# Kernel tuning notes

Measured on AMD Instinct MI355X. Metric: run time of the kernel, lower is better.

## Reference

```python
import jax, jax.numpy as jnp
import numpy as np

B, I, H, O = 4096, 1024, 2048, 512  # batch, input_size, experts_out(hidden), experts_hidden(output)
E_SPEC, E_SH = 4, 4


def _experts(x, W1, b1, W2, b2):
    # x:[B,I], W1:[E,I,H], b1:[E,H], W2:[E,H,O], b2:[E,O] -> [E,B,O]
    # Expert: fc2(dropout(relu(fc1(x)))); dropout is identity in eval mode.
    h = jax.nn.relu(jnp.einsum('bi,eih->ebh', x, W1) + b1[:, None, :])
    return jnp.einsum('ebh,eho->ebo', h, W2) + b2[:, None, :]


def setup_inputs() -> dict:
    key = jax.random.key(0)
    ks = jax.random.split(key, 32)
    s = 0.02
    d = {}
    d['x_shared'] = jax.random.normal(ks[0], (B, I), jnp.float32)
    d['x_task1'] = jax.random.normal(ks[1], (B, I), jnp.float32)
    d['x_task2'] = jax.random.normal(ks[2], (B, I), jnp.float32)
    # expert params for shared / task1 / task2 groups
    for n, (grp, kbase) in enumerate([('sh', 3), ('t1', 8), ('t2', 13)]):
        E = E_SH if grp == 'sh' else E_SPEC
        d[f'w1_{grp}'] = jax.random.normal(ks[kbase], (E, I, H), jnp.float32) * s
        d[f'b1_{grp}'] = jnp.zeros((E, H), jnp.float32)
        d[f'w2_{grp}'] = jax.random.normal(ks[kbase + 1], (E, H, O), jnp.float32) * s
        d[f'b2_{grp}'] = jnp.zeros((E, O), jnp.float32)
    # gate params
    d['wg_sh'] = jax.random.normal(ks[20], (I, 2 * E_SPEC + E_SH), jnp.float32) * s
    d['bg_sh'] = jnp.zeros((2 * E_SPEC + E_SH,), jnp.float32)
    d['wg_t1'] = jax.random.normal(ks[21], (I, E_SPEC + E_SH), jnp.float32) * s
    d['bg_t1'] = jnp.zeros((E_SPEC + E_SH,), jnp.float32)
    d['wg_t2'] = jax.random.normal(ks[22], (I, E_SPEC + E_SH), jnp.float32) * s
    d['bg_t2'] = jnp.zeros((E_SPEC + E_SH,), jnp.float32)
    return d


def reference(x_shared, x_task1, x_task2,
              w1_sh, b1_sh, w2_sh, b2_sh,
              w1_t1, b1_t1, w2_t1, b2_t1,
              w1_t2, b1_t2, w2_t2, b2_t2,
              wg_sh, bg_sh, wg_t1, bg_t1, wg_t2, bg_t2):
    sh_o = _experts(x_shared, w1_sh, b1_sh, w2_sh, b2_sh)  # [Esh,B,O]
    t1_o = _experts(x_task1, w1_t1, b1_t1, w2_t1, b2_t1)   # [Esp,B,O]
    t2_o = _experts(x_task2, w1_t2, b1_t2, w2_t2, b2_t2)   # [Esp,B,O]

    g1 = jax.nn.softmax(x_task1 @ wg_t1 + bg_t1, axis=1)    # [B,Esp+Esh]
    g2 = jax.nn.softmax(x_task2 @ wg_t2 + bg_t2, axis=1)
    gs = jax.nn.softmax(x_shared @ wg_sh + bg_sh, axis=1)   # [B,2Esp+Esh]

    out1 = jnp.einsum('ebc,be->bc', jnp.concatenate([t1_o, sh_o], 0), g1)
    out2 = jnp.einsum('ebc,be->bc', jnp.concatenate([t2_o, sh_o], 0), g2)
    out_sh = jnp.einsum('ebc,be->bc', jnp.concatenate([t1_o, t2_o, sh_o], 0), gs)
    # if_last=False -> return [shared, task1, task2]
    return (out_sh, out1, out2)
```

## Files before the change

### kernel.cpp

```cpp
#include <hip/hip_runtime.h>

#define B_DIM 4096
#define I_DIM 1024
#define H_DIM 2048
#define O_DIM 512

typedef unsigned short ushort_t;
typedef unsigned long long ull_t;
typedef __attribute__((ext_vector_type(4))) float f32x4;
typedef __attribute__((ext_vector_type(8))) short bf16x8;
typedef __attribute__((ext_vector_type(8))) unsigned short u16x8;
typedef __attribute__((ext_vector_type(4))) unsigned short u16x4;

__device__ __forceinline__ unsigned short f2bf(float f) {
  union { float f; unsigned int u; } v; v.f = f;
  unsigned int u = v.u;
  u += 0x7fffu + ((u >> 16) & 1u);
  return (unsigned short)(u >> 16);
}
__device__ __forceinline__ float bf2f(unsigned short h) {
  union { unsigned int u; float f; } v; v.u = ((unsigned int)h) << 16;
  return v.f;
}

__device__ __forceinline__ void gld16(const void* g, void* l) {
  __builtin_amdgcn_global_load_lds(
      (const __attribute__((address_space(1))) unsigned int*)((ull_t)g),
      (__attribute__((address_space(3))) unsigned int*)((unsigned int)(ull_t)l),
      16, 0, 0);
}

__device__ __forceinline__ int swz_off(int row, int col) {
  int off = ((((row >> 4) << 1) + (col >> 5)) << 10) + ((row & 15) << 6) + ((col & 31) << 1);
  off ^= ((row >> 3) & 1) << 5;
  return off;
}

template <bool RELU, int WM, int WN, int MR, int NR>
__device__ __forceinline__ void gemm_core(
    const ushort_t* __restrict__ A,
    const ushort_t* __restrict__ Bt,
    const float*    __restrict__ bias,
    ushort_t*       __restrict__ C,
    int N, int K, int bm0, int bn0)
{
  constexpr int BM = WM * MR * 16;
  constexpr int BN = WN * NR * 16;
  constexpr int CA = BM / 64;
  constexpr int CB = BN / 64;
  constexpr int NTH = WM * WN * 64;
  constexpr int MH = MR / 2, NH = NR / 2;
  constexpr int ABYTES = BM * 128;
  constexpr int BBYTES = BN * 128;
  constexpr int VM = CA + CB;

  __shared__ __align__(16) char lds[2 * (ABYTES + BBYTES)];

  const int tid  = threadIdx.x;
  const int lane = tid & 63;
  const int wave = tid >> 6;
  const int wm = wave / WN, wn = wave % WN;
  const int r16 = lane & 15, kq = lane >> 4;

  int loffA[CA]; ull_t goffA[CA];
  int loffB[CB]; ull_t goffB[CB];
#pragma unroll
  for (int r = 0; r < CA; ++r) {
    const int L = (r * NTH + tid) * 16;
    const int P = L ^ (((L >> 9) & 1) << 5);
    const int s = P >> 10;
    const int row = ((s >> 1) << 4) | ((P >> 6) & 15);
    const int col = ((s & 1) << 5) | (((P >> 4) & 3) << 3);
    loffA[r] = L;
    goffA[r] = (ull_t)(bm0 + row) * K + col;
  }
#pragma unroll
  for (int r = 0; r < CB; ++r) {
    const int L = (r * NTH + tid) * 16;
    const int P = L ^ (((L >> 9) & 1) << 5);
    const int s = P >> 10;
    const int row = ((s >> 1) << 4) | ((P >> 6) & 15);
    const int col = ((s & 1) << 5) | (((P >> 4) & 3) << 3);
    loffB[r] = L;
    goffB[r] = (ull_t)(bn0 + row) * K + col;
  }
  const int NT = K >> 6;

  int offA[MR][2], offB[NR][2];
#pragma unroll
  for (int m = 0; m < MR; ++m)
#pragma unroll
    for (int ks = 0; ks < 2; ++ks)
      offA[m][ks] = swz_off(wm * MR * 16 + m * 16 + r16, ks * 32 + kq * 8);
#pragma unroll
  for (int n = 0; n < NR; ++n)
#pragma unroll
    for (int ks = 0; ks < 2; ++ks)
      offB[n][ks] = swz_off(wn * NR * 16 + n * 16 + r16, ks * 32 + kq * 8);

  f32x4 acc[MR][NR] = {};

  auto stageA = [&](int b, int kt) {
    char* base = lds + b * (ABYTES + BBYTES);
    const int k0 = kt << 6;
#pragma unroll
    for (int r = 0; r < CA; ++r) gld16(A + goffA[r] + k0, base + loffA[r]);
  };
  auto stageB = [&](int b, int kt) {
    char* base = lds + b * (ABYTES + BBYTES) + ABYTES;
    const int k0 = kt << 6;
#pragma unroll
    for (int r = 0; r < CB; ++r) gld16(Bt + goffB[r] + k0, base + loffB[r]);
  };

  stageA(0, 0); stageB(0, 0);
  stageA(1, 1); stageB(1, 1);

  for (int kt = 0; kt < NT; ++kt) {
    const int b = kt & 1;
    const bool pre = (kt + 2 < NT);
    if (kt < NT - 1) {
      if constexpr (VM == 8)      asm volatile("s_waitcnt vmcnt(8)" ::: "memory");
      else if constexpr (VM == 6) asm volatile("s_waitcnt vmcnt(6)" ::: "memory");
      else                        asm volatile("s_waitcnt vmcnt(0)" ::: "memory");
    } else                        asm volatile("s_waitcnt vmcnt(0)" ::: "memory");
    __builtin_amdgcn_s_barrier();

    const char* tA = lds + b * (ABYTES + BBYTES);
    const char* tB = tA + ABYTES;

    bf16x8 a_lo[MH][2], a_hi[MH][2], b_lo[NH][2], b_hi[NH][2];

#pragma unroll
    for (int m = 0; m < MH; ++m) {
      a_lo[m][0] = *(const bf16x8*)(tA + offA[m][0]);
      a_lo[m][1] = *(const bf16x8*)(tA + offA[m][1]);
    }
#pragma unroll
    for (int n = 0; n < NH; ++n) {
      b_lo[n][0] = *(const bf16x8*)(tB + offB[n][0]);
      b_lo[n][1] = *(const bf16x8*)(tB + offB[n][1]);
    }
    asm volatile("s_waitcnt lgkmcnt(0)" ::: "memory");
    __builtin_amdgcn_sched_barrier(0);
    __builtin_amdgcn_s_setprio(1);
#pragma unroll
    for (int m = 0; m < MH; ++m)
#pragma unroll
      for (int n = 0; n < NH; ++n)
#pragma unroll
        for (int ks = 0; ks < 2; ++ks)
          acc[m][n] = __builtin_amdgcn_mfma_f32_16x16x32_bf16(a_lo[m][ks], b_lo[n][ks], acc[m][n], 0, 0, 0);
    __builtin_amdgcn_s_setprio(0);

#pragma unroll
    for (int n = 0; n < NH; ++n) {
      b_hi[n][0] = *(const bf16x8*)(tB + offB[n + NH][0]);
      b_hi[n][1] = *(const bf16x8*)(tB + offB[n + NH][1]);
    }
    asm volatile("s_waitcnt lgkmcnt(0)" ::: "memory");
    __builtin_amdgcn_sched_barrier(0);
    __builtin_amdgcn_s_setprio(1);
#pragma unroll
    for (int m = 0; m < MH; ++m)
#pragma unroll
      for (int n = 0; n < NH; ++n)
#pragma unroll
        for (int ks = 0; ks < 2; ++ks)
          acc[m][n + NH] = __builtin_amdgcn_mfma_f32_16x16x32_bf16(a_lo[m][ks], b_hi[n][ks], acc[m][n + NH], 0, 0, 0);
    __builtin_amdgcn_s_setprio(0);
    asm volatile("" ::: "memory");
    __builtin_amdgcn_s_barrier();

#pragma unroll
    for (int m = 0; m < MH; ++m) {
      a_hi[m][0] = *(const bf16x8*)(tA + offA[m + MH][0]);
      a_hi[m][1] = *(const bf16x8*)(tA + offA[m + MH][1]);
    }
    if (pre) stageB(b, kt + 2);
    asm volatile("s_waitcnt lgkmcnt(0)" ::: "memory");
    __builtin_amdgcn_sched_barrier(0);
    __builtin_amdgcn_s_setprio(1);
#pragma unroll
    for (int m = 0; m < MH; ++m)
#pragma unroll
      for (int n = 0; n < NH; ++n)
#pragma unroll
        for (int ks = 0; ks < 2; ++ks)
          acc[m + MH][n + NH] = __builtin_amdgcn_mfma_f32_16x16x32_bf16(a_hi[m][ks], b_hi[n][ks], acc[m + MH][n + NH], 0, 0, 0);
    __builtin_amdgcn_s_setprio(0);
    asm volatile("" ::: "memory");
    __builtin_amdgcn_s_barrier();

    if (pre) stageA(b, kt + 2);
    __builtin_amdgcn_sched_barrier(0);
    __builtin_amdgcn_s_setprio(1);
#pragma unroll
    for (int m = 0; m < MH; ++m)
#pragma unroll
      for (int n = 0; n < NH; ++n)
#pragma unroll
        for (int ks = 0; ks < 2; ++ks)
          acc[m + MH][n] = __builtin_amdgcn_mfma_f32_16x16x32_bf16(a_hi[m][ks], b_lo[n][ks], acc[m + MH][n], 0, 0, 0);
    __builtin_amdgcn_s_setprio(0);
  }

  float bv[NR];
#pragma unroll
  for (int n = 0; n < NR; ++n) bv[n] = bias[bn0 + wn * NR * 16 + n * 16 + r16];
#pragma unroll
  for (int m = 0; m < MR; ++m) {
    const int row = bm0 + wm * MR * 16 + m * 16 + kq * 4;
#pragma unroll
    for (int n = 0; n < NR; ++n) {
      const int col = bn0 + wn * NR * 16 + n * 16 + r16;
#pragma unroll
      for (int j = 0; j < 4; ++j) {
        float v = acc[m][n][j] + bv[n];
        if (RELU) v = fmaxf(v, 0.f);
        C[(ull_t)(row + j) * N + col] = f2bf(v);
      }
    }
  }
}

__device__ __forceinline__ void xcd_swz(int& bx, int& by, int& bz) {
  const int gx = gridDim.x, gy = gridDim.y;
  const int total = gx * gy * gridDim.z;
  const int flat = blockIdx.x + gx * (blockIdx.y + gy * blockIdx.z);
  const int q = total >> 3;
  const int s = (flat & 7) * q + (flat >> 3);
  bx = s % gx;
  const int rest = s / gx;
  by = rest % gy;
  bz = rest / gy;
}

__global__ __launch_bounds__(512, 2) void gemm1_256_kernel(
    const ushort_t* __restrict__ xb,
    const ushort_t* __restrict__ w1t,
    const float* __restrict__ b1_t1, const float* __restrict__ b1_t2, const float* __restrict__ b1_sh,
    ushort_t* __restrict__ hbuf,
    int ebase)
{
  int bx, by, bz; xcd_swz(bx, by, bz);
  const int eg = ebase + bz;
  const ushort_t* A  = xb + (ull_t)(eg >> 2) * B_DIM * I_DIM;
  const ushort_t* Bt = w1t + (ull_t)bz * H_DIM * I_DIM;
  const float* bias = (eg < 4 ? b1_t1 : eg < 8 ? b1_t2 : b1_sh) + (ull_t)(eg & 3) * H_DIM;
  ushort_t* C = hbuf + (ull_t)bz * B_DIM * H_DIM;
  gemm_core<true, 2, 4, 8, 4>(A, Bt, bias, C, H_DIM, I_DIM, by * 256, bx * 256);
}

__global__ __launch_bounds__(512, 2) void gemm2_256_kernel(
    const ushort_t* __restrict__ hbuf,
    const ushort_t* __restrict__ w2t,
    const float* __restrict__ b2_t1, const float* __restrict__ b2_t2, const float* __restrict__ b2_sh,
    ushort_t* __restrict__ eout,
    int ebase)
{
  int bx, by, bz; xcd_swz(bx, by, bz);
  const int eg = ebase + bz;
  const ushort_t* A  = hbuf + (ull_t)bz * B_DIM * H_DIM;
  const ushort_t* Bt = w2t + (ull_t)bz * O_DIM * H_DIM;
  const float* bias = (eg < 4 ? b2_t1 : eg < 8 ? b2_t2 : b2_sh) + (ull_t)(eg & 3) * O_DIM;
  ushort_t* C = eout + (ull_t)eg * B_DIM * O_DIM;
  gemm_core<false, 4, 2, 4, 4>(A, Bt, bias, C, O_DIM, H_DIM, by * 256, bx * 128);
}

__global__ void tcast64_kernel(const float* __restrict__ s_t1, const float* __restrict__ s_t2,
                               const float* __restrict__ s_sh, ushort_t* __restrict__ dst,
                               int R, int C, int ebase)
{
  __shared__ float tile[64][33];
  const int eg = ebase + blockIdx.z;
  const float* src = (eg < 4 ? s_t1 : eg < 8 ? s_t2 : s_sh) + (ull_t)(eg & 3) * R * C;
  ushort_t* d = dst + (ull_t)blockIdx.z * R * C;
  const int tx = threadIdx.x, ty = threadIdx.y;
  const int r0 = blockIdx.y * 64, c0 = blockIdx.x * 32;
#pragma unroll
  for (int i = 0; i < 64; i += 8)
    tile[i + ty][tx] = src[(ull_t)(r0 + i + ty) * C + c0 + tx];
  __syncthreads();
  const int tid = ty * 32 + tx;
  const int c = tid >> 3, q = tid & 7;
  u16x8 rv;
#pragma unroll
  for (int k = 0; k < 8; ++k) rv[k] = f2bf(tile[q * 8 + k][c]);
  *(u16x8*)(d + (ull_t)(c0 + c) * R + r0 + q * 8) = rv;
}

__global__ void cast_x_kernel(const float* __restrict__ xt1, const float* __restrict__ xt2,
                              const float* __restrict__ xsh, ushort_t* __restrict__ dst)
{
  const int slot = blockIdx.y;
  const float* src = slot == 0 ? xt1 : slot == 1 ? xt2 : xsh;
  const ull_t base = ((ull_t)blockIdx.x * 256 + threadIdx.x) * 8;
  const f32x4* s4 = (const f32x4*)(src + base);
  f32x4 a = s4[0], b = s4[1];
  u16x8 r;
  r[0] = f2bf(a[0]); r[1] = f2bf(a[1]); r[2] = f2bf(a[2]); r[3] = f2bf(a[3]);
  r[4] = f2bf(b[0]); r[5] = f2bf(b[1]); r[6] = f2bf(b[2]); r[7] = f2bf(b[3]);
  *(u16x8*)(dst + (ull_t)slot * B_DIM * I_DIM + base) = r;
}

__global__ void prep_gates_w_kernel(const float* __restrict__ wg_sh, const float* __restrict__ wg_t1,
                                    const float* __restrict__ wg_t2, ushort_t* __restrict__ wgtb)
{
  const int t = blockIdx.x;
  const float* src = t == 0 ? wg_sh : t == 1 ? wg_t1 : wg_t2;
  const int n = t == 0 ? 12 : 8;
  ushort_t* dst = wgtb + (ull_t)t * 16 * I_DIM;
  for (int i = threadIdx.x; i < 16 * (I_DIM / 8); i += blockDim.x) {
    const int c = i >> 7, j0 = (i & 127) * 8;
    u16x8 r;
#pragma unroll
    for (int k = 0; k < 8; ++k)
      r[k] = (c < n) ? f2bf(src[(ull_t)(j0 + k) * n + c]) : (ushort_t)0;
    *(u16x8*)(dst + (ull_t)c * I_DIM + j0) = r;
  }
}

__global__ __launch_bounds__(256, 2) void gates_mfma_kernel(
    const ushort_t* __restrict__ xb, const ushort_t* __restrict__ wgtb,
    const float* __restrict__ bg_sh, const float* __restrict__ bg_t1, const float* __restrict__ bg_t2,
    float* __restrict__ gates)
{
  __shared__ __align__(16) ushort_t As[128 * 32];
  const int task = blockIdx.y;
  const int slot = task == 0 ? 2 : task - 1;
  const int n = task == 0 ? 12 : 8;
  const float* bg = task == 0 ? bg_sh : task == 1 ? bg_t1 : bg_t2;
  float* out = task == 0 ? gates
             : task == 1 ? gates + (ull_t)B_DIM * 12
                         : gates + (ull_t)B_DIM * 20;
  const ushort_t* A  = xb + (ull_t)slot * B_DIM * I_DIM;
  const ushort_t* Bt = wgtb + (ull_t)task * 16 * I_DIM;

  const int tid = threadIdx.x, lane = tid & 63, wave = tid >> 6;
  const int brow = blockIdx.x * 128;
  const int r16 = lane & 15, kq = lane >> 4;

  f32x4 acc[2] = {};
  const int c0 = tid, c1 = tid + 256;
  const ull_t a_off0 = (ull_t)(brow + (c0 >> 2)) * I_DIM + (c0 & 3) * 8;
  const ull_t a_off1 = (ull_t)(brow + (c1 >> 2)) * I_DIM + (c1 & 3) * 8;

  for (int k0 = 0; k0 < I_DIM; k0 += 32) {
    gld16(A + a_off0 + k0, As + c0 * 8);
    gld16(A + a_off1 + k0, As + c1 * 8);
    __syncthreads();
    const bf16x8 bfr = *(const bf16x8*)(Bt + (ull_t)r16 * I_DIM + k0 + kq * 8);
    const bf16x8 af0 = *(const bf16x8*)(As + (wave * 32 + r16) * 32 + kq * 8);
    const bf16x8 af1 = *(const bf16x8*)(As + (wave * 32 + 16 + r16) * 32 + kq * 8);
    acc[0] = __builtin_amdgcn_mfma_f32_16x16x32_bf16(af0, bfr, acc[0], 0, 0, 0);
    acc[1] = __builtin_amdgcn_mfma_f32_16x16x32_bf16(af1, bfr, acc[1], 0, 0, 0);
    __syncthreads();
  }

  const float bv = (r16 < n) ? bg[r16] : 0.f;
#pragma unroll
  for (int m = 0; m < 2; ++m) {
#pragma unroll
    for (int j = 0; j < 4; ++j) {
      float v = (r16 < n) ? (acc[m][j] + bv) : -1e30f;
      float mx = v;
#pragma unroll
      for (int d = 1; d < 16; d <<= 1) mx = fmaxf(mx, __shfl_xor(mx, d));
      const float e = __expf(v - mx);
      float s = e;
#pragma unroll
      for (int d = 1; d < 16; d <<= 1) s += __shfl_xor(s, d);
      const int row = brow + wave * 32 + m * 16 + kq * 4 + j;
      if (r16 < n) out[(ull_t)row * n + r16] = e / s;
    }
  }
}

__global__ __launch_bounds__(256) void combine_kernel(
    const ushort_t* __restrict__ eout, const float* __restrict__ gates, float* __restrict__ out)
{
  const ull_t idx4 = (ull_t)blockIdx.x * 256 + threadIdx.x;
  const int b  = (int)(idx4 >> 7);
  const int o4 = ((int)idx4 & 127) * 4;
  const float* gs = gates + (ull_t)b * 12;
  const float* g1 = gates + (ull_t)B_DIM * 12 + (ull_t)b * 8;
  const float* g2 = gates + (ull_t)B_DIM * 20 + (ull_t)b * 8;
  float osh[4] = {0, 0, 0, 0}, o1[4] = {0, 0, 0, 0}, o2[4] = {0, 0, 0, 0};
#pragma unroll
  for (int j = 0; j < 12; ++j) {
    const u16x4 ev = *(const u16x4*)(eout + ((ull_t)j * B_DIM + b) * O_DIM + o4);
    const float wsh = gs[j];
    const float w1 = (j < 4) ? g1[j] : (j >= 8 ? g1[j - 4] : 0.f);
    const float w2 = (j < 4) ? 0.f : g2[j - 4];
#pragma unroll
    for (int t = 0; t < 4; ++t) {
      const float e = bf2f(ev[t]);
      osh[t] += wsh * e; o1[t] += w1 * e; o2[t] += w2 * e;
    }
  }
  const ull_t nBO = (ull_t)B_DIM * O_DIM;
  const ull_t obase = (ull_t)b * O_DIM + o4;
  f32x4 v0 = {osh[0], osh[1], osh[2], osh[3]};
  f32x4 v1 = {o1[0], o1[1], o1[2], o1[3]};
  f32x4 v2 = {o2[0], o2[1], o2[2], o2[3]};
  *(f32x4*)(out + obase) = v0;
  *(f32x4*)(out + nBO + obase) = v1;
  *(f32x4*)(out + 2 * nBO + obase) = v2;
}

extern "C" void kernel_launch(void* const* d_in, const int* in_sizes, int n_in,
                              void* d_out, int out_size, void* d_ws, size_t ws_size,
                              hipStream_t stream)
{
  const float* x_sh  = (const float*)d_in[0];
  const float* x_t1  = (const float*)d_in[1];
  const float* x_t2  = (const float*)d_in[2];
  const float* w1_sh = (const float*)d_in[3];
  const float* b1_sh = (const float*)d_in[4];
  const float* w2_sh = (const float*)d_in[5];
  const float* b2_sh = (const float*)d_in[6];
  const float* w1_t1 = (const float*)d_in[7];
  const float* b1_t1 = (const float*)d_in[8];
  const float* w2_t1 = (const float*)d_in[9];
  const float* b2_t1 = (const float*)d_in[10];
  const float* w1_t2 = (const float*)d_in[11];
  const float* b1_t2 = (const float*)d_in[12];
  const float* w2_t2 = (const float*)d_in[13];
  const float* b2_t2 = (const float*)d_in[14];
  const float* wg_sh = (const float*)d_in[15];
  const float* bg_sh = (const float*)d_in[16];
  const float* wg_t1 = (const float*)d_in[17];
  const float* bg_t1 = (const float*)d_in[18];
  const float* wg_t2 = (const float*)d_in[19];
  const float* bg_t2 = (const float*)d_in[20];

  char* p = (char*)d_ws;
  auto alloc = [&](size_t bytes) { char* r = p; p += (bytes + 255) & ~(size_t)255; return r; };

  ushort_t* xb    = (ushort_t*)alloc(3ull * B_DIM * I_DIM * 2);
  ushort_t* eout  = (ushort_t*)alloc(12ull * B_DIM * O_DIM * 2);
  float*    gates = (float*)alloc(28ull * B_DIM * 4);
  ushort_t* wgtb  = (ushort_t*)alloc(3ull * 16 * I_DIM * 2);

  const size_t used_fixed = (size_t)(p - (char*)d_ws);
  const size_t per_e = ((size_t)H_DIM * I_DIM + (size_t)O_DIM * H_DIM + (size_t)B_DIM * H_DIM) * 2 + 3 * 256;
  int eb = 1;
  if (ws_size > used_fixed + per_e) eb = (int)((ws_size - used_fixed) / per_e);
  if (eb > 12) eb = 12;
  if (eb < 1)  eb = 1;

  ushort_t* w1t  = (ushort_t*)alloc((size_t)eb * H_DIM * I_DIM * 2);
  ushort_t* w2t  = (ushort_t*)alloc((size_t)eb * O_DIM * H_DIM * 2);
  ushort_t* hbuf = (ushort_t*)alloc((size_t)eb * B_DIM * H_DIM * 2);

  cast_x_kernel<<<dim3(2048, 3), 256, 0, stream>>>(x_t1, x_t2, x_sh, xb);
  prep_gates_w_kernel<<<3, 256, 0, stream>>>(wg_sh, wg_t1, wg_t2, wgtb);
  gates_mfma_kernel<<<dim3(B_DIM / 128, 3), 256, 0, stream>>>(xb, wgtb, bg_sh, bg_t1, bg_t2, gates);
  for (int ebase = 0; ebase < 12; ebase += eb) {
    const int cnt = (12 - ebase < eb) ? (12 - ebase) : eb;
    tcast64_kernel<<<dim3(H_DIM / 32, I_DIM / 64, cnt), dim3(32, 8), 0, stream>>>(
        w1_t1, w1_t2, w1_sh, w1t, I_DIM, H_DIM, ebase);
    tcast64_kernel<<<dim3(O_DIM / 32, H_DIM / 64, cnt), dim3(32, 8), 0, stream>>>(
        w2_t1, w2_t2, w2_sh, w2t, H_DIM, O_DIM, ebase);
    gemm1_256_kernel<<<dim3(H_DIM / 256, B_DIM / 256, cnt), 512, 0, stream>>>(
        xb, w1t, b1_t1, b1_t2, b1_sh, hbuf, ebase);
    gemm2_256_kernel<<<dim3(O_DIM / 128, B_DIM / 256, cnt), 512, 0, stream>>>(
        hbuf, w2t, b2_t1, b2_t2, b2_sh, eout, ebase);
  }
  combine_kernel<<<dim3((B_DIM * O_DIM / 4) / 256), 256, 0, stream>>>(eout, gates, (float*)d_out);
}
```

Before: 416.1 us.

## Retile gemm2 to 128x128, merge prefetch stages, simplify gates and widen combine

Changes several unrelated things at once. gemm2 moves to 128x128 tiles with 256-thread blocks, giving more blocks for the small-N second GEMM, and the per-thread load counts are now derived from tile bytes. In the shared GEMM core, one mid-iteration barrier is removed and both the A and B prefetches are issued together after the final barrier. The gates kernel drops its LDS staging and loads MFMA operands straight from global memory with two accumulators, and the combine kernel processes 8 elements per thread. The trade-off is less compute/load overlap inside each K-tile, in return for fewer barriers and better occupancy of the second GEMM.

Measured after the change: 414.5 us. No clear change (-0.4%).

```diff
diff --git a/kernel.cpp b/kernel.cpp
--- a/kernel.cpp
+++ b/kernel.cpp
@@ -46,12 +46,12 @@
 {
   constexpr int BM = WM * MR * 16;
   constexpr int BN = WN * NR * 16;
-  constexpr int CA = BM / 64;
-  constexpr int CB = BN / 64;
   constexpr int NTH = WM * WN * 64;
   constexpr int MH = MR / 2, NH = NR / 2;
   constexpr int ABYTES = BM * 128;
   constexpr int BBYTES = BN * 128;
+  constexpr int CA = ABYTES / (NTH * 16);
+  constexpr int CB = BBYTES / (NTH * 16);
   constexpr int VM = CA + CB;
 
   __shared__ __align__(16) char lds[2 * (ABYTES + BBYTES)];
@@ -120,10 +120,11 @@
     const int b = kt & 1;
     const bool pre = (kt + 2 < NT);
     if (kt < NT - 1) {
-      if constexpr (VM == 8)      asm volatile("s_waitcnt vmcnt(8)" ::: "memory");
-      else if constexpr (VM == 6) asm volatile("s_waitcnt vmcnt(6)" ::: "memory");
-      else                        asm volatile("s_waitcnt vmcnt(0)" ::: "memory");
-    } else                        asm volatile("s_waitcnt vmcnt(0)" ::: "memory");
+      static_assert(VM == 8, "vmcnt literal assumes 8 loads/K-tile/thread");
+      asm volatile("s_waitcnt vmcnt(8)" ::: "memory");
+    } else {
+      asm volatile("s_waitcnt vmcnt(0)" ::: "memory");
+    }
     __builtin_amdgcn_s_barrier();
 
     const char* tA = lds + b * (ABYTES + BBYTES);
@@ -169,15 +170,12 @@
         for (int ks = 0; ks < 2; ++ks)
           acc[m][n + NH] = __builtin_amdgcn_mfma_f32_16x16x32_bf16(a_lo[m][ks], b_hi[n][ks], acc[m][n + NH], 0, 0, 0);
     __builtin_amdgcn_s_setprio(0);
-    asm volatile("" ::: "memory");
-    __builtin_amdgcn_s_barrier();
 
 #pragma unroll
     for (int m = 0; m < MH; ++m) {
       a_hi[m][0] = *(const bf16x8*)(tA + offA[m + MH][0]);
       a_hi[m][1] = *(const bf16x8*)(tA + offA[m + MH][1]);
     }
-    if (pre) stageB(b, kt + 2);
     asm volatile("s_waitcnt lgkmcnt(0)" ::: "memory");
     __builtin_amdgcn_sched_barrier(0);
     __builtin_amdgcn_s_setprio(1);
@@ -192,7 +190,7 @@
     asm volatile("" ::: "memory");
     __builtin_amdgcn_s_barrier();
 
-    if (pre) stageA(b, kt + 2);
+    if (pre) { stageB(b, kt + 2); stageA(b, kt + 2); }
     __builtin_amdgcn_sched_barrier(0);
     __builtin_amdgcn_s_setprio(1);
 #pragma unroll
@@ -252,7 +250,7 @@
   gemm_core<true, 2, 4, 8, 4>(A, Bt, bias, C, H_DIM, I_DIM, by * 256, bx * 256);
 }
 
-__global__ __launch_bounds__(512, 2) void gemm2_256_kernel(
+__global__ __launch_bounds__(256, 2) void gemm2_128_kernel(
     const ushort_t* __restrict__ hbuf,
     const ushort_t* __restrict__ w2t,
     const float* __restrict__ b2_t1, const float* __restrict__ b2_t2, const float* __restrict__ b2_sh,
@@ -265,7 +263,7 @@
   const ushort_t* Bt = w2t + (ull_t)bz * O_DIM * H_DIM;
   const float* bias = (eg < 4 ? b2_t1 : eg < 8 ? b2_t2 : b2_sh) + (ull_t)(eg & 3) * O_DIM;
   ushort_t* C = eout + (ull_t)eg * B_DIM * O_DIM;
-  gemm_core<false, 4, 2, 4, 4>(A, Bt, bias, C, O_DIM, H_DIM, by * 256, bx * 128);
+  gemm_core<false, 2, 2, 4, 4>(A, Bt, bias, C, O_DIM, H_DIM, by * 128, bx * 128);
 }
 
 __global__ void tcast64_kernel(const float* __restrict__ s_t1, const float* __restrict__ s_t2,
@@ -321,12 +319,11 @@
   }
 }
 
-__global__ __launch_bounds__(256, 2) void gates_mfma_kernel(
+__global__ __launch_bounds__(256) void gates_direct_kernel(
     const ushort_t* __restrict__ xb, const ushort_t* __restrict__ wgtb,
     const float* __restrict__ bg_sh, const float* __restrict__ bg_t1, const float* __restrict__ bg_t2,
     float* __restrict__ gates)
 {
-  __shared__ __align__(16) ushort_t As[128 * 32];
   const int task = blockIdx.y;
   const int slot = task == 0 ? 2 : task - 1;
   const int n = task == 0 ? 12 : 8;
@@ -334,79 +331,74 @@
   float* out = task == 0 ? gates
              : task == 1 ? gates + (ull_t)B_DIM * 12
                          : gates + (ull_t)B_DIM * 20;
-  const ushort_t* A  = xb + (ull_t)slot * B_DIM * I_DIM;
-  const ushort_t* Bt = wgtb + (ull_t)task * 16 * I_DIM;
-
-  const int tid = threadIdx.x, lane = tid & 63, wave = tid >> 6;
-  const int brow = blockIdx.x * 128;
+
+  const int lane = threadIdx.x & 63, wave = threadIdx.x >> 6;
   const int r16 = lane & 15, kq = lane >> 4;
-
-  f32x4 acc[2] = {};
-  const int c0 = tid, c1 = tid + 256;
-  const ull_t a_off0 = (ull_t)(brow + (c0 >> 2)) * I_DIM + (c0 & 3) * 8;
-  const ull_t a_off1 = (ull_t)(brow + (c1 >> 2)) * I_DIM + (c1 & 3) * 8;
-
-  for (int k0 = 0; k0 < I_DIM; k0 += 32) {
-    gld16(A + a_off0 + k0, As + c0 * 8);
-    gld16(A + a_off1 + k0, As + c1 * 8);
-    __syncthreads();
-    const bf16x8 bfr = *(const bf16x8*)(Bt + (ull_t)r16 * I_DIM + k0 + kq * 8);
-    const bf16x8 af0 = *(const bf16x8*)(As + (wave * 32 + r16) * 32 + kq * 8);
-    const bf16x8 af1 = *(const bf16x8*)(As + (wave * 32 + 16 + r16) * 32 + kq * 8);
-    acc[0] = __builtin_amdgcn_mfma_f32_16x16x32_bf16(af0, bfr, acc[0], 0, 0, 0);
-    acc[1] = __builtin_amdgcn_mfma_f32_16x16x32_bf16(af1, bfr, acc[1], 0, 0, 0);
-    __syncthreads();
+  const int brow = blockIdx.x * 64 + wave * 16;
+
+  const ushort_t* Arow = xb + (ull_t)slot * B_DIM * I_DIM + (ull_t)(brow + r16) * I_DIM + kq * 8;
+  const ushort_t* Brow = wgtb + (ull_t)task * 16 * I_DIM + (ull_t)r16 * I_DIM + kq * 8;
+
+  f32x4 acc0 = {}, acc1 = {};
+#pragma unroll
+  for (int k0 = 0; k0 < I_DIM; k0 += 64) {
+    const bf16x8 a0 = *(const bf16x8*)(Arow + k0);
+    const bf16x8 b0 = *(const bf16x8*)(Brow + k0);
+    const bf16x8 a1 = *(const bf16x8*)(Arow + k0 + 32);
+    const bf16x8 b1 = *(const bf16x8*)(Brow + k0 + 32);
+    acc0 = __builtin_amdgcn_mfma_f32_16x16x32_bf16(a0, b0, acc0, 0, 0, 0);
+    acc1 = __builtin_amdgcn_mfma_f32_16x16x32_bf16(a1, b1, acc1, 0, 0, 0);
   }
 
   const float bv = (r16 < n) ? bg[r16] : 0.f;
 #pragma unroll
-  for (int m = 0; m < 2; ++m) {
-#pragma unroll
-    for (int j = 0; j < 4; ++j) {
-      float v = (r16 < n) ? (acc[m][j] + bv) : -1e30f;
-      float mx = v;
-#pragma unroll
-      for (int d = 1; d < 16; d <<= 1) mx = fmaxf(mx, __shfl_xor(mx, d));
-      const float e = __expf(v - mx);
-      float s = e;
-#pragma unroll
-      for (int d = 1; d < 16; d <<= 1) s += __shfl_xor(s, d);
-      const int row = brow + wave * 32 + m * 16 + kq * 4 + j;
-      if (r16 < n) out[(ull_t)row * n + r16] = e / s;
-    }
+  for (int j = 0; j < 4; ++j) {
+    float v = (r16 < n) ? (acc0[j] + acc1[j] + bv) : -1e30f;
+    float mx = v;
+#pragma unroll
+    for (int d = 1; d < 16; d <<= 1) mx = fmaxf(mx, __shfl_xor(mx, d));
+    const float e = __expf(v - mx);
+    float s = e;
+#pragma unroll
+    for (int d = 1; d < 16; d <<= 1) s += __shfl_xor(s, d);
+    const int row = brow + kq * 4 + j;
+    if (r16 < n) out[(ull_t)row * n + r16] = e / s;
   }
 }
 
 __global__ __launch_bounds__(256) void combine_kernel(
     const ushort_t* __restrict__ eout, const float* __restrict__ gates, float* __restrict__ out)
 {
-  const ull_t idx4 = (ull_t)blockIdx.x * 256 + threadIdx.x;
-  const int b  = (int)(idx4 >> 7);
-  const int o4 = ((int)idx4 & 127) * 4;
+  const ull_t idx8 = (ull_t)blockIdx.x * 256 + threadIdx.x;
+  const int b  = (int)(idx8 >> 6);
+  const int o8 = ((int)idx8 & 63) * 8;
   const float* gs = gates + (ull_t)b * 12;
   const float* g1 = gates + (ull_t)B_DIM * 12 + (ull_t)b * 8;
   const float* g2 = gates + (ull_t)B_DIM * 20 + (ull_t)b * 8;
-  float osh[4] = {0, 0, 0, 0}, o1[4] = {0, 0, 0, 0}, o2[4] = {0, 0, 0, 0};
+  float osh[8] = {}, o1[8] = {}, o2[8] = {};
 #pragma unroll
   for (int j = 0; j < 12; ++j) {
-    const u16x4 ev = *(const u16x4*)(eout + ((ull_t)j * B_DIM + b) * O_DIM + o4);
+    const u16x8 ev = *(const u16x8*)(eout + ((ull_t)j * B_DIM + b) * O_DIM + o8);
     const float wsh = gs[j];
     const float w1 = (j < 4) ? g1[j] : (j >= 8 ? g1[j - 4] : 0.f);
-    const float w2 = (j < 4) ? 0.f : g2[j - 4];
-#pragma unroll
-    for (int t = 0; t < 4; ++t) {
+    const float w2 = (j < 4) ? 0.f : (j < 8 ? g2[j - 4] : g2[j - 4]);
+#pragma unroll
+    for (int t = 0; t < 8; ++t) {
       const float e = bf2f(ev[t]);
       osh[t] += wsh * e; o1[t] += w1 * e; o2[t] += w2 * e;
     }
   }
   const ull_t nBO = (ull_t)B_DIM * O_DIM;
-  const ull_t obase = (ull_t)b * O_DIM + o4;
-  f32x4 v0 = {osh[0], osh[1], osh[2], osh[3]};
-  f32x4 v1 = {o1[0], o1[1], o1[2], o1[3]};
-  f32x4 v2 = {o2[0], o2[1], o2[2], o2[3]};
-  *(f32x4*)(out + obase) = v0;
-  *(f32x4*)(out + nBO + obase) = v1;
-  *(f32x4*)(out + 2 * nBO + obase) = v2;
+  const ull_t obase = (ull_t)b * O_DIM + o8;
+#pragma unroll
+  for (int h = 0; h < 2; ++h) {
+    f32x4 v0 = {osh[h*4], osh[h*4+1], osh[h*4+2], osh[h*4+3]};
+    f32x4 v1 = {o1[h*4], o1[h*4+1], o1[h*4+2], o1[h*4+3]};
+    f32x4 v2 = {o2[h*4], o2[h*4+1], o2[h*4+2], o2[h*4+3]};
+    *(f32x4*)(out + obase + h*4) = v0;
+    *(f32x4*)(out + nBO + obase + h*4) = v1;
+    *(f32x4*)(out + 2 * nBO + obase + h*4) = v2;
+  }
 }
 
 extern "C" void kernel_launch(void* const* d_in, const int* in_sizes, int n_in,
@@ -456,7 +448,7 @@
 
   cast_x_kernel<<<dim3(2048, 3), 256, 0, stream>>>(x_t1, x_t2, x_sh, xb);
   prep_gates_w_kernel<<<3, 256, 0, stream>>>(wg_sh, wg_t1, wg_t2, wgtb);
-  gates_mfma_kernel<<<dim3(B_DIM / 128, 3), 256, 0, stream>>>(xb, wgtb, bg_sh, bg_t1, bg_t2, gates);
+  gates_direct_kernel<<<dim3(B_DIM / 64, 3), 256, 0, stream>>>(xb, wgtb, bg_sh, bg_t1, bg_t2, gates);
   for (int ebase = 0; ebase < 12; ebase += eb) {
     const int cnt = (12 - ebase < eb) ? (12 - ebase) : eb;
     tcast64_kernel<<<dim3(H_DIM / 32, I_DIM / 64, cnt), dim3(32, 8), 0, stream>>>(
@@ -465,8 +457,8 @@
         w2_t1, w2_t2, w2_sh, w2t, H_DIM, O_DIM, ebase);
     gemm1_256_kernel<<<dim3(H_DIM / 256, B_DIM / 256, cnt), 512, 0, stream>>>(
         xb, w1t, b1_t1, b1_t2, b1_sh, hbuf, ebase);
-    gemm2_256_kernel<<<dim3(O_DIM / 128, B_DIM / 256, cnt), 512, 0, stream>>>(
+    gemm2_128_kernel<<<dim3(O_DIM / 128, B_DIM / 128, cnt), 256, 0, stream>>>(
         hbuf, w2t, b2_t1, b2_t2, b2_sh, eout, ebase);
   }
-  combine_kernel<<<dim3((B_DIM * O_DIM / 4) / 256), 256, 0, stream>>>(eout, gates, (float*)d_out);
-}
+  combine_kernel<<<dim3((B_DIM * O_DIM / 8) / 256), 256, 0, stream>>>(eout, gates, (float*)d_out);
+}
```
